# Kernel tuning notes

Hardware: AMD Instinct MI355X
Metric: run time of the kernel (lower is better)

The kernel has to match this reference:

```python
import jax, jax.numpy as jnp
import numpy as np

N_NODES = 10000
N_EDGES = 160000
F_IN = 256
HEADS = 4
F_OUT = 256
NEG_SLOPE = 0.2  # PyG GATConv default negative_slope
EPS = 1e-5       # GraphNorm eps


def gat_conv(x, src, dst, W, a_src, a_dst, bias, concat):
    """PyG-style GATConv. x:[N,Fin], W:[Fin,H*C], a_src/a_dst:[H,C], bias:[H*C] or [C].
    src/dst already include self-loops (add_self_loops=True default)."""
    N = x.shape[0]
    H, C = a_src.shape
    h = (x @ W).reshape(N, H, C)                      # per-head projected features
    al_s = jnp.einsum('nhc,hc->nh', h, a_src)          # [N,H]
    al_d = jnp.einsum('nhc,hc->nh', h, a_dst)          # [N,H]
    e = jax.nn.leaky_relu(al_s[src] + al_d[dst], NEG_SLOPE)  # [E,H] raw scores
    # segment softmax over edges grouped by destination node
    m = jax.ops.segment_max(e, dst, num_segments=N)    # [N,H]; every node has a self-loop
    ex = jnp.exp(e - m[dst])
    denom = jax.ops.segment_sum(ex, dst, num_segments=N)
    alpha = ex / denom[dst]                            # [E,H]
    out = jax.ops.segment_sum(h[src] * alpha[:, :, None], dst, num_segments=N)  # [N,H,C]
    out = out.reshape(N, H * C) if concat else out.mean(axis=1)
    return out + bias


def graph_norm(x, w, b, ms):
    """PyG GraphNorm over a single graph: y = w*(x-ms*mean)/sqrt(var+eps)+b."""
    mean = x.mean(axis=0, keepdims=True)
    sh = x - ms * mean
    var = (sh * sh).mean(axis=0, keepdims=True)
    return w * sh / jnp.sqrt(var + EPS) + b


def setup_inputs() -> dict:
    key = jax.random.key(0)
    ks = jax.random.split(key, 12)
    H1 = HEADS * F_IN  # 1024
    s = 0.05
    return {
        'x': jax.random.normal(ks[0], (N_NODES, F_IN), jnp.float32),
        'edge_index': jax.random.randint(ks[1], (2, N_EDGES), 0, N_NODES, jnp.int64),
        'W1': jax.random.normal(ks[2], (F_IN, HEADS * F_IN), jnp.float32) * s,
        'att_src1': jax.random.normal(ks[3], (HEADS, F_IN), jnp.float32) * s,
        'att_dst1': jax.random.normal(ks[4], (HEADS, F_IN), jnp.float32) * s,
        'b1': jnp.zeros((H1,), jnp.float32),
        'gn_w': jnp.ones((H1,), jnp.float32),
        'gn_b': jnp.zeros((H1,), jnp.float32),
        'gn_ms': jnp.ones((H1,), jnp.float32),
        'W2': jax.random.normal(ks[5], (H1, F_OUT), jnp.float32) * s,
        'att_src2': jax.random.normal(ks[6], (1, F_OUT), jnp.float32) * s,
        'att_dst2': jax.random.normal(ks[7], (1, F_OUT), jnp.float32) * s,
        'b2': jnp.zeros((F_OUT,), jnp.float32),
    }


def reference(x, edge_index, W1, att_src1, att_dst1, b1, gn_w, gn_b, gn_ms,
              W2, att_src2, att_dst2, b2):
    N = x.shape[0]
    loop = jnp.arange(N, dtype=edge_index.dtype)
    src = jnp.concatenate([edge_index[0], loop])  # add_self_loops=True
    dst = jnp.concatenate([edge_index[1], loop])
    h = gat_conv(x, src, dst, W1, att_src1, att_dst1, b1, concat=True)   # [N, H*Fin]
    h = graph_norm(h, gn_w, gn_b, gn_ms)
    h = jax.nn.relu(h)
    # F.dropout(training=self.training): eval mode -> identity
    out = gat_conv(h, src, dst, W2, att_src2, att_dst2, b2, concat=False)  # [N, Fout]
    return out
```

## Files before the change

### kernel.cpp

```cpp
#include <hip/hip_runtime.h>
#include <hip/hip_bf16.h>

#define NNODES 10000
#define FIN    256
#define HEADS  4
#define H1DIM  1024
#define FOUT   256
#define NEG    0.2f
#define GNEPS  1e-5f
#define SLOTS  96

typedef unsigned short u16;
typedef __attribute__((ext_vector_type(8))) short bf16x8;
typedef __attribute__((ext_vector_type(4))) float f32x4;

__device__ __forceinline__ float bf2f(u16 u) {
    union { unsigned int i; float f; } v; v.i = ((unsigned int)u) << 16; return v.f;
}
__device__ __forceinline__ u16 f2bf(float f) {
    __hip_bfloat16 h = __float2bfloat16(f);
    union { __hip_bfloat16 h; u16 u; } v; v.h = h; return v.u;
}
__device__ __forceinline__ float lrelu(float v) { return v > 0.f ? v : NEG * v; }

__device__ __forceinline__ void compute_flags(const int* ei, const u16* x,
                                              int& is64, int& isbf)
{
    int or_odd = ei[1] | ei[3] | ei[5] | ei[7] | ei[9] | ei[11];
    is64 = (or_odd == 0) ? 1 : 0;
    int sane = 1;
    for (int i = 0; i < 32; i += 2) {
        u16 w = x[i];
        int e = (w >> 7) & 0xFF;
        if (!(w == 0 || w == 0x8000 || (e >= 100 && e <= 150))) sane = 0;
    }
    isbf = sane;
}

struct CvtDesc { const void* src; float* dst; int n; };
struct CvtTable { CvtDesc d[9]; };

__global__ void prep_kernel(const void* __restrict__ x, const int* __restrict__ ei,
                            const void* __restrict__ W1, const void* __restrict__ W2,
                            const void* __restrict__ as1, const void* __restrict__ ad1,
                            CvtTable smalls,
                            u16* __restrict__ xb, u16* __restrict__ W1t,
                            u16* __restrict__ W2t, float* __restrict__ Pm,
                            int* __restrict__ cursor, int* __restrict__ ssort,
                            int* __restrict__ flag, int* __restrict__ fflag,
                            int NE, int Etot)
{
    __shared__ int sfl[2];
    __shared__ u16 tile[32][33];
    if (threadIdx.x == 0) {
        int is64, isbf;
        compute_flags(ei, (const u16*)x, is64, isbf);
        sfl[0] = is64; sfl[1] = isbf;
        if (blockIdx.y == 3 && blockIdx.x == 0) { flag[0] = is64; fflag[0] = isbf; }
    }
    __syncthreads();
    const int is64 = sfl[0], isbf = sfl[1];
    const int task = blockIdx.y;
    const int tid = threadIdx.x;

    if (task == 0) {
        int i4 = (blockIdx.x * 256 + tid) * 4;
        if (i4 >= NNODES * FIN) return;
        if (isbf) {
            *reinterpret_cast<ushort4*>(xb + i4) =
                *reinterpret_cast<const ushort4*>((const u16*)x + i4);
        } else {
            float4 v = *reinterpret_cast<const float4*>((const float*)x + i4);
            ushort4 o; o.x = f2bf(v.x); o.y = f2bf(v.y); o.z = f2bf(v.z); o.w = f2bf(v.w);
            *reinterpret_cast<ushort4*>(xb + i4) = o;
        }
    } else if (task == 1 || task == 2) {
        const void* W = (task == 1) ? W1 : W2;
        u16* Wt = (task == 1) ? W1t : W2t;
        const int K = (task == 1) ? FIN : H1DIM;
        const int N = (task == 1) ? H1DIM : FOUT;
        int ntiles_n = N >> 5;
        int tk = blockIdx.x / ntiles_n, tn = blockIdx.x - tk * ntiles_n;
        if (tk >= (K >> 5)) return;
        int k0 = tk << 5, n0 = tn << 5;
        int r = tid >> 5, cdx = tid & 31;
#pragma unroll
        for (int i = 0; i < 4; i++) {
            int kk = i * 8 + r;
            int srcIdx = (k0 + kk) * N + n0 + cdx;
            u16 v = isbf ? ((const u16*)W)[srcIdx] : f2bf(((const float*)W)[srcIdx]);
            tile[kk][cdx] = v;
        }
        __syncthreads();
#pragma unroll
        for (int i = 0; i < 4; i++) {
            int nn = i * 8 + r;
            Wt[(size_t)(n0 + nn) * K + k0 + cdx] = tile[cdx][nn];
        }
    } else if (task == 3) {
        if (blockIdx.x >= 9) return;
        CvtDesc d = smalls.d[blockIdx.x];
        int i4 = tid * 4;
        if (i4 >= d.n) return;
        if (isbf) {
            ushort4 u = *reinterpret_cast<const ushort4*>((const u16*)d.src + i4);
            *reinterpret_cast<float4*>(d.dst + i4) =
                make_float4(bf2f(u.x), bf2f(u.y), bf2f(u.z), bf2f(u.w));
        } else {
            *reinterpret_cast<float4*>(d.dst + i4) =
                *reinterpret_cast<const float4*>((const float*)d.src + i4);
        }
    } else if (task == 4) {
        int e = blockIdx.x * 256 + tid;
        if (e >= Etot) return;
        int src, dst;
        if (e < NE) {
            src = is64 ? ei[2 * e] : ei[e];
            dst = is64 ? ei[2 * (NE + e)] : ei[NE + e];
        } else {
            src = dst = e - NE;
        }
        if ((unsigned)dst >= NNODES) return;
        if ((unsigned)src >= NNODES) src = 0;
        int idx = atomicAdd(&cursor[dst], 1);
        if (idx < SLOTS) ssort[dst * SLOTS + idx] = src;
    } else {
        if (blockIdx.x >= 512) return;
        int wave = tid >> 6, lane = tid & 63;
        int idx = blockIdx.x * 4 + wave;
        int j = idx >> 8, k = idx & 255;
        int hd = j & 3;
        const void* av = (j < 4) ? as1 : ad1;
        int c = lane * 4;
        int widx = k * H1DIM + hd * FIN + c;
        int aidx = hd * FIN + c;
        float wv0, wv1, wv2, wv3, a0, a1, a2, a3;
        if (isbf) {
            ushort4 wu = *reinterpret_cast<const ushort4*>((const u16*)W1 + widx);
            ushort4 au = *reinterpret_cast<const ushort4*>((const u16*)av + aidx);
            wv0 = bf2f(wu.x); wv1 = bf2f(wu.y); wv2 = bf2f(wu.z); wv3 = bf2f(wu.w);
            a0 = bf2f(au.x); a1 = bf2f(au.y); a2 = bf2f(au.z); a3 = bf2f(au.w);
        } else {
            float4 wf = *reinterpret_cast<const float4*>((const float*)W1 + widx);
            float4 af = *reinterpret_cast<const float4*>((const float*)av + aidx);
            wv0 = wf.x; wv1 = wf.y; wv2 = wf.z; wv3 = wf.w;
            a0 = af.x; a1 = af.y; a2 = af.z; a3 = af.w;
        }
        float acc = wv0 * a0 + wv1 * a1 + wv2 * a2 + wv3 * a3;
#pragma unroll
        for (int off = 32; off > 0; off >>= 1)
            acc += __shfl_xor(acc, off, 64);
        if (lane == 0) Pm[j * FIN + k] = acc;
    }
}

__global__ void alsd1_kernel(const u16* __restrict__ xb, const float* __restrict__ Pm,
                             float* __restrict__ als, float* __restrict__ ald)
{
    int wave = threadIdx.x >> 6, lane = threadIdx.x & 63;
    int n = blockIdx.x * 4 + wave;
    if (n >= NNODES) return;
    ushort4 xv = *reinterpret_cast<const ushort4*>(xb + (size_t)n * FIN + lane * 4);
    float x0 = bf2f(xv.x), x1 = bf2f(xv.y), x2 = bf2f(xv.z), x3 = bf2f(xv.w);
    float r[8];
#pragma unroll
    for (int j = 0; j < 8; j++) {
        float4 p = *reinterpret_cast<const float4*>(Pm + j * FIN + lane * 4);
        r[j] = x0 * p.x + x1 * p.y + x2 * p.z + x3 * p.w;
    }
#pragma unroll
    for (int off = 32; off > 0; off >>= 1)
#pragma unroll
        for (int j = 0; j < 8; j++)
            r[j] += __shfl_xor(r[j], off, 64);
    if (lane == 0) {
        *reinterpret_cast<float4*>(als + n * 4) = make_float4(r[0], r[1], r[2], r[3]);
        *reinterpret_cast<float4*>(ald + n * 4) = make_float4(r[4], r[5], r[6], r[7]);
    }
}

__global__ void agg_x_kernel(const int* __restrict__ cursor, const int* __restrict__ ssort,
                             const float* __restrict__ als, const float* __restrict__ ald,
                             const u16* __restrict__ xb, u16* __restrict__ zbuf)
{
    const int wave = threadIdx.x >> 6, lane = threadIdx.x & 63;
    const int n = blockIdx.x * 4 + wave;
    const bool active = (n < NNODES);
    int e0 = 0, e1 = 0;
    float4 adv = make_float4(0.f, 0.f, 0.f, 0.f);
    if (active) {
        e0 = n * SLOTS;
        e1 = e0 + min(cursor[n], SLOTS);
        adv = *reinterpret_cast<const float4*>(ald + n * 4);
    }

    float m0 = -1e30f, m1 = -1e30f, m2 = -1e30f, m3 = -1e30f;
    for (int e = e0 + lane; e < e1; e += 64) {
        int s = ssort[e];
        float4 av = *reinterpret_cast<const float4*>(als + s * 4);
        m0 = fmaxf(m0, lrelu(av.x + adv.x));
        m1 = fmaxf(m1, lrelu(av.y + adv.y));
        m2 = fmaxf(m2, lrelu(av.z + adv.z));
        m3 = fmaxf(m3, lrelu(av.w + adv.w));
    }
#pragma unroll
    for (int off = 32; off > 0; off >>= 1) {
        m0 = fmaxf(m0, __shfl_xor(m0, off, 64));
        m1 = fmaxf(m1, __shfl_xor(m1, off, 64));
        m2 = fmaxf(m2, __shfl_xor(m2, off, 64));
        m3 = fmaxf(m3, __shfl_xor(m3, off, 64));
    }

    __shared__ float wlds[4][128][4];
    __shared__ int schk[4];
    int myCh = active ? ((e1 - e0 + 127) >> 7) : 0;
    if (lane == 0) schk[wave] = myCh;
    __syncthreads();
    int mc = max(max(schk[0], schk[1]), max(schk[2], schk[3]));

    float d0 = 0, d1 = 0, d2 = 0, d3 = 0;
    float a[4][4];
#pragma unroll
    for (int h = 0; h < 4; h++)
#pragma unroll
        for (int c = 0; c < 4; c++) a[h][c] = 0.f;

    for (int ch = 0; ch < mc; ch++) {
        int cs = e0 + ch * 128;
        int ce = min(cs + 128, e1);
        if (ch < myCh) {
            for (int e = cs + lane; e < ce; e += 64) {
                int s = ssort[e];
                float4 av = *reinterpret_cast<const float4*>(als + s * 4);
                float w0 = __expf(lrelu(av.x + adv.x) - m0);
                float w1 = __expf(lrelu(av.y + adv.y) - m1);
                float w2 = __expf(lrelu(av.z + adv.z) - m2);
                float w3 = __expf(lrelu(av.w + adv.w) - m3);
                *reinterpret_cast<float4*>(&wlds[wave][e - cs][0]) = make_float4(w0, w1, w2, w3);
                d0 += w0; d1 += w1; d2 += w2; d3 += w3;
            }
        }
        __syncthreads();
        if (ch < myCh) {
            for (int ee = cs; ee < ce; ee++) {
                int s = ssort[ee];
                float4 w = *reinterpret_cast<const float4*>(&wlds[wave][ee - cs][0]);
                ushort4 xv = *reinterpret_cast<const ushort4*>(xb + (size_t)s * FIN + lane * 4);
                float x0 = bf2f(xv.x), x1 = bf2f(xv.y), x2 = bf2f(xv.z), x3 = bf2f(xv.w);
                a[0][0] += w.x * x0; a[0][1] += w.x * x1; a[0][2] += w.x * x2; a[0][3] += w.x * x3;
                a[1][0] += w.y * x0; a[1][1] += w.y * x1; a[1][2] += w.y * x2; a[1][3] += w.y * x3;
                a[2][0] += w.z * x0; a[2][1] += w.z * x1; a[2][2] += w.z * x2; a[2][3] += w.z * x3;
                a[3][0] += w.w * x0; a[3][1] += w.w * x1; a[3][2] += w.w * x2; a[3][3] += w.w * x3;
            }
        }
        __syncthreads();
    }
    if (!active) return;
#pragma unroll
    for (int off = 32; off > 0; off >>= 1) {
        d0 += __shfl_xor(d0, off, 64);
        d1 += __shfl_xor(d1, off, 64);
        d2 += __shfl_xor(d2, off, 64);
        d3 += __shfl_xor(d3, off, 64);
    }
    float invs[4];
    invs[0] = d0 > 0.f ? 1.f / d0 : 0.f;
    invs[1] = d1 > 0.f ? 1.f / d1 : 0.f;
    invs[2] = d2 > 0.f ? 1.f / d2 : 0.f;
    invs[3] = d3 > 0.f ? 1.f / d3 : 0.f;
#pragma unroll
    for (int h = 0; h < 4; h++) {
        ushort4 o;
        o.x = f2bf(a[h][0] * invs[h]);
        o.y = f2bf(a[h][1] * invs[h]);
        o.z = f2bf(a[h][2] * invs[h]);
        o.w = f2bf(a[h][3] * invs[h]);
        *reinterpret_cast<ushort4*>(zbuf + (size_t)h * NNODES * FIN + (size_t)n * FIN + lane * 4) = o;
    }
}

#define LDS_STRIDE 40
#define KCHUNK2 512
template<int BN, int MINW, bool NORM_A, bool BIAS, bool SPLITK, bool STATS>
__global__ void __launch_bounds__(256, MINW)
mfma_gemm(const u16* __restrict__ A, const u16* __restrict__ Bt,
          u16* __restrict__ C, float* __restrict__ Cf,
          const float* __restrict__ bias,
          float* __restrict__ gsum, float* __restrict__ gsum2,
          const float* __restrict__ gnw, const float* __restrict__ gnb,
          const float* __restrict__ gnms,
          int M, int K, int ldc, long aZ, long bZ, int cZ, int kChunk)
{
    constexpr int NI = BN / 32;
    constexpr int NLOADS = (512 + BN * 4) / 256;
    __shared__ u16 Alds[128 * LDS_STRIDE];
    __shared__ u16 Blds[BN * LDS_STRIDE];
    __shared__ float sc_lds[NORM_A ? KCHUNK2 : 1];
    __shared__ float sh_lds[NORM_A ? KCHUNK2 : 1];

    const u16* Az; const u16* Bz; int k0;
    if (SPLITK) { Az = A; Bz = Bt; k0 = blockIdx.z * kChunk; }
    else { Az = A + (long)blockIdx.z * aZ; Bz = Bt + (long)blockIdx.z * bZ; k0 = 0; }
    const int kEnd = k0 + kChunk;

    const int tid  = threadIdx.x;
    const int lane = tid & 63;
    const int wave = tid >> 6;
    const int wm = wave >> 1, wn = wave & 1;
    const int l15 = lane & 15, quad = lane >> 4;
    const int n0 = blockIdx.x * BN;
    const int m0 = blockIdx.y * 128;

    if (NORM_A) {
        const float invN = 1.0f / (float)NNODES;
        for (int i = tid; i < kChunk; i += 256) {
            int cch = k0 + i;
            float mean = gsum[cch] * invN;
            float ex2  = gsum2[cch] * invN;
            float msv  = gnms[cch];
            float var  = ex2 - 2.f * msv * mean * mean + msv * msv * mean * mean;
            float sc   = gnw[cch] * rsqrtf(fmaxf(var, 0.f) + GNEPS);
            sc_lds[i] = sc;
            sh_lds[i] = gnb[cch] - sc * msv * mean;
        }
        __syncthreads();
    }

    int lrow[NLOADS], lcol[NLOADS];
    bool lIsA[NLOADS];
#pragma unroll
    for (int i = 0; i < NLOADS; i++) {
        int g = i * 256 + tid;
        lIsA[i] = g < 512;
        int gg = lIsA[i] ? g : g - 512;
        lrow[i] = gg >> 2;
        lcol[i] = (gg & 3) * 8;
    }
    uint4 pre[NLOADS];

    auto issue = [&](int kt) {
#pragma unroll
        for (int i = 0; i < NLOADS; i++) {
            if (lIsA[i]) {
                int gr = m0 + lrow[i];
                pre[i] = (gr < M)
                    ? *reinterpret_cast<const uint4*>(Az + (size_t)gr * K + kt + lcol[i])
                    : make_uint4(0u, 0u, 0u, 0u);
            } else {
                pre[i] = *reinterpret_cast<const uint4*>(Bz + (size_t)(n0 + lrow[i]) * K + kt + lcol[i]);
            }
        }
    };
    auto commit = [&](int kt) {
#pragma unroll
        for (int i = 0; i < NLOADS; i++) {
            uint4 v = pre[i];
            if (lIsA[i]) {
                if (NORM_A) {
                    int kr = kt - k0 + lcol[i];
                    float4 s0 = *reinterpret_cast<const float4*>(&sc_lds[kr]);
                    float4 s1 = *reinterpret_cast<const float4*>(&sc_lds[kr + 4]);
                    float4 h0 = *reinterpret_cast<const float4*>(&sh_lds[kr]);
                    float4 h1 = *reinterpret_cast<const float4*>(&sh_lds[kr + 4]);
                    float sc[8] = {s0.x, s0.y, s0.z, s0.w, s1.x, s1.y, s1.z, s1.w};
                    float sh[8] = {h0.x, h0.y, h0.z, h0.w, h1.x, h1.y, h1.z, h1.w};
                    u16* pv = reinterpret_cast<u16*>(&v);
#pragma unroll
                    for (int j = 0; j < 8; j++)
                        pv[j] = f2bf(fmaxf(0.f, bf2f(pv[j]) * sc[j] + sh[j]));
                }
                *reinterpret_cast<uint4*>(&Alds[lrow[i] * LDS_STRIDE + lcol[i]]) = v;
            } else {
                *reinterpret_cast<uint4*>(&Blds[lrow[i] * LDS_STRIDE + lcol[i]]) = v;
            }
        }
    };

    f32x4 acc[4][NI];
#pragma unroll
    for (int i = 0; i < 4; i++)
#pragma unroll
        for (int j = 0; j < NI; j++) acc[i][j] = (f32x4){0.f, 0.f, 0.f, 0.f};

    issue(k0);
    for (int kt = k0; kt < kEnd; kt += 32) {
        commit(kt);
        __syncthreads();
        if (kt + 32 < kEnd) issue(kt + 32);

        bf16x8 a_frag[4], b_frag[NI];
#pragma unroll
        for (int mi = 0; mi < 4; mi++)
            a_frag[mi] = *reinterpret_cast<const bf16x8*>(
                &Alds[(wm * 64 + mi * 16 + l15) * LDS_STRIDE + quad * 8]);
#pragma unroll
        for (int ni = 0; ni < NI; ni++)
            b_frag[ni] = *reinterpret_cast<const bf16x8*>(
                &Blds[(wn * (BN / 2) + ni * 16 + l15) * LDS_STRIDE + quad * 8]);
#pragma unroll
        for (int mi = 0; mi < 4; mi++)
#pragma unroll
            for (int ni = 0; ni < NI; ni++)
                acc[mi][ni] = __builtin_amdgcn_mfma_f32_16x16x32_bf16(
                    a_frag[mi], b_frag[ni], acc[mi][ni], 0, 0, 0);
        __syncthreads();
    }

    float sacc[NI], qacc[NI];
#pragma unroll
    for (int ni = 0; ni < NI; ni++) { sacc[ni] = 0.f; qacc[ni] = 0.f; }

#pragma unroll
    for (int mi = 0; mi < 4; mi++) {
#pragma unroll
        for (int r = 0; r < 4; r++) {
            int row = m0 + wm * 64 + mi * 16 + quad * 4 + r;
            if (row >= M) continue;
#pragma unroll
            for (int ni = 0; ni < NI; ni++) {
                int col = n0 + wn * (BN / 2) + ni * 16 + l15;
                float v = acc[mi][ni][r];
                if (SPLITK) {
                    Cf[(size_t)blockIdx.z * M * ldc + (size_t)row * ldc + col] = v;
                } else {
                    if (BIAS) v += bias[blockIdx.z * cZ + col];
                    if (STATS) { sacc[ni] += v; qacc[ni] += v * v; }
                    C[(size_t)row * ldc + blockIdx.z * cZ + col] = f2bf(v);
                }
            }
        }
    }
    if (STATS) {
#pragma unroll
        for (int ni = 0; ni < NI; ni++) {
            float s = sacc[ni], q = qacc[ni];
            s += __shfl_xor(s, 16, 64); q += __shfl_xor(q, 16, 64);
            s += __shfl_xor(s, 32, 64); q += __shfl_xor(q, 32, 64);
            if (quad == 0) {
                int ch = blockIdx.z * cZ + n0 + wn * (BN / 2) + ni * 16 + l15;
                atomicAdd(&gsum[ch], s);
                atomicAdd(&gsum2[ch], q);
            }
        }
    }
}

__global__ void h2fin_kernel(const float* __restrict__ h2p, u16* __restrict__ h2b,
                             const float* __restrict__ as, const float* __restrict__ ad,
                             float* __restrict__ als, float* __restrict__ ald)
{
    int wave = threadIdx.x >> 6, lane = threadIdx.x & 63;
    int n = blockIdx.x * 4 + wave;
    if (n >= NNODES) return;
    int c = lane * 4;
    float4 v0 = *reinterpret_cast<const float4*>(h2p + (size_t)n * FOUT + c);
    float4 v1 = *reinterpret_cast<const float4*>(h2p + (size_t)NNODES * FOUT + (size_t)n * FOUT + c);
    float4 v = make_float4(v0.x + v1.x, v0.y + v1.y, v0.z + v1.z, v0.w + v1.w);
    ushort4 o; o.x = f2bf(v.x); o.y = f2bf(v.y); o.z = f2bf(v.z); o.w = f2bf(v.w);
    *reinterpret_cast<ushort4*>(h2b + (size_t)n * FOUT + c) = o;
    float4 av = *reinterpret_cast<const float4*>(as + c);
    float4 dv = *reinterpret_cast<const float4*>(ad + c);
    float ps = v.x * av.x + v.y * av.y + v.z * av.z + v.w * av.w;
    float pd = v.x * dv.x + v.y * dv.y + v.z * dv.z + v.w * dv.w;
#pragma unroll
    for (int off = 32; off > 0; off >>= 1) {
        ps += __shfl_xor(ps, off, 64);
        pd += __shfl_xor(pd, off, 64);
    }
    if (lane == 0) { als[n] = ps; ald[n] = pd; }
}

__global__ void agg2_kernel(const int* __restrict__ cursor, const int* __restrict__ ssort,
                            const float* __restrict__ als, const float* __restrict__ ald,
                            const u16* __restrict__ h2, const float* __restrict__ b2,
                            const int* __restrict__ fflag, void* __restrict__ outv)
{
    const int wave = threadIdx.x >> 6, lane = threadIdx.x & 63;
    const int n = blockIdx.x * 4 + wave;
    const bool active = (n < NNODES);
    int e0 = 0, e1 = 0;
    float adv = 0.f;
    if (active) {
        e0 = n * SLOTS;
        e1 = e0 + min(cursor[n], SLOTS);
        adv = ald[n];
    }

    float m = -1e30f;
    for (int e = e0 + lane; e < e1; e += 64) {
        int s = ssort[e];
        m = fmaxf(m, lrelu(als[s] + adv));
    }
#pragma unroll
    for (int off = 32; off > 0; off >>= 1)
        m = fmaxf(m, __shfl_xor(m, off, 64));

    __shared__ float wlds[4][128];
    __shared__ int schk[4];
    int myCh = active ? ((e1 - e0 + 127) >> 7) : 0;
    if (lane == 0) schk[wave] = myCh;
    __syncthreads();
    int mc = max(max(schk[0], schk[1]), max(schk[2], schk[3]));

    float d = 0.f, a0 = 0.f, a1 = 0.f, a2 = 0.f, a3 = 0.f;
    for (int ch = 0; ch < mc; ch++) {
        int cs = e0 + ch * 128;
        int ce = min(cs + 128, e1);
        if (ch < myCh) {
            for (int e = cs + lane; e < ce; e += 64) {
                int s = ssort[e];
                float w = __expf(lrelu(als[s] + adv) - m);
                wlds[wave][e - cs] = w;
                d += w;
            }
        }
        __syncthreads();
        if (ch < myCh) {
            for (int ee = cs; ee < ce; ee++) {
                int s = ssort[ee];
                float w = wlds[wave][ee - cs];
                ushort4 hv = *reinterpret_cast<const ushort4*>(h2 + (size_t)s * FOUT + lane * 4);
                a0 += w * bf2f(hv.x); a1 += w * bf2f(hv.y);
                a2 += w * bf2f(hv.z); a3 += w * bf2f(hv.w);
            }
        }
        __syncthreads();
    }
    if (!active) return;
#pragma unroll
    for (int off = 32; off > 0; off >>= 1)
        d += __shfl_xor(d, off, 64);
    float inv = d > 0.f ? 1.f / d : 0.f;
    int c = lane * 4;
    float4 bv = *reinterpret_cast<const float4*>(b2 + c);
    float r0 = a0 * inv + bv.x;
    float r1 = a1 * inv + bv.y;
    float r2 = a2 * inv + bv.z;
    float r3 = a3 * inv + bv.w;
    if (fflag[0]) {
        ushort4 o;
        o.x = f2bf(r0); o.y = f2bf(r1); o.z = f2bf(r2); o.w = f2bf(r3);
        *reinterpret_cast<ushort4*>((u16*)outv + (size_t)n * FOUT + c) = o;
    } else {
        *reinterpret_cast<float4*>((float*)outv + (size_t)n * FOUT + c) =
            make_float4(r0, r1, r2, r3);
    }
}

extern "C" void kernel_launch(void* const* d_in, const int* in_sizes, int n_in,
                              void* d_out, int out_size, void* d_ws, size_t ws_size,
                              hipStream_t stream)
{
    const void* x    = d_in[0];
    const int*  ei   = (const int*)d_in[1];
    const void* W1   = d_in[2];
    const void* as1  = d_in[3];
    const void* ad1  = d_in[4];
    const void* b1   = d_in[5];
    const void* gnw  = d_in[6];
    const void* gnb  = d_in[7];
    const void* gnms = d_in[8];
    const void* W2   = d_in[9];
    const void* as2  = d_in[10];
    const void* ad2  = d_in[11];
    const void* b2   = d_in[12];

    const int NE   = in_sizes[1] / 2;
    const int Etot = NE + NNODES;

    char* w = (char*)d_ws;
    size_t off = 0;
    auto carve = [&](size_t bytes) -> char* {
        char* p = w + off;
        off = (off + bytes + 255) & ~(size_t)255;
        return p;
    };
    int*   cursor = (int*)carve((size_t)NNODES * 4);
    float* gsum   = (float*)carve(1024 * 4);
    float* gsum2  = (float*)carve(1024 * 4);
    size_t zero_bytes = off;
    int*   flag   = (int*)carve(256);
    int*   fflag  = (int*)carve(256);
    int*   ssort  = (int*)carve((size_t)NNODES * SLOTS * 4);
    u16*   zbuf   = (u16*)carve((size_t)HEADS * NNODES * FIN * 2);
    u16*   out1b  = (u16*)carve((size_t)NNODES * H1DIM * 2);
    float* al1s   = (float*)carve((size_t)NNODES * HEADS * 4);
    float* al1d   = (float*)carve((size_t)NNODES * HEADS * 4);
    float* al2s   = (float*)carve((size_t)NNODES * 4);
    float* al2d   = (float*)carve((size_t)NNODES * 4);
    u16*   xb     = (u16*)carve((size_t)NNODES * FIN * 2);
    u16*   W1t    = (u16*)carve((size_t)H1DIM * FIN * 2);
    u16*   W2t    = (u16*)carve((size_t)FOUT * H1DIM * 2);
    float* Pm     = (float*)carve(8 * FIN * 4);
    float* b1f    = (float*)carve(1024 * 4);
    float* gnwf   = (float*)carve(1024 * 4);
    float* gnbf   = (float*)carve(1024 * 4);
    float* gnmsf  = (float*)carve(1024 * 4);
    float* as2f   = (float*)carve(256 * 4);
    float* ad2f   = (float*)carve(256 * 4);
    float* b2f    = (float*)carve(256 * 4);
    float* as1f   = (float*)carve(1024 * 4);
    float* ad1f   = (float*)carve(1024 * 4);
    (void)ws_size;

    float* h2part = (float*)zbuf;
    u16*   h2b    = xb;

    hipMemsetAsync(d_ws, 0, zero_bytes, stream);

    {
        CvtTable tab;
        tab.d[0] = { b1,   b1f,   H1DIM };
        tab.d[1] = { gnw,  gnwf,  H1DIM };
        tab.d[2] = { gnb,  gnbf,  H1DIM };
        tab.d[3] = { gnms, gnmsf, H1DIM };
        tab.d[4] = { as2,  as2f,  FOUT };
        tab.d[5] = { ad2,  ad2f,  FOUT };
        tab.d[6] = { b2,   b2f,   FOUT };
        tab.d[7] = { as1,  as1f,  H1DIM };
        tab.d[8] = { ad1,  ad1f,  H1DIM };
        dim3 grd(2500, 6);
        prep_kernel<<<grd, 256, 0, stream>>>(x, ei, W1, W2, as1, ad1, tab,
                                             xb, W1t, W2t, Pm, cursor, ssort,
                                             flag, fflag, NE, Etot);
    }
    alsd1_kernel<<<2500, 256, 0, stream>>>(xb, Pm, al1s, al1d);
    agg_x_kernel<<<2500, 256, 0, stream>>>(cursor, ssort, al1s, al1d, xb, zbuf);
    {
        dim3 grd(FIN / 128, (NNODES + 127) / 128, HEADS);
        mfma_gemm<128, 2, false, true, false, true><<<grd, 256, 0, stream>>>(
            zbuf, W1t, out1b, nullptr, b1f, gsum, gsum2, nullptr, nullptr, nullptr,
            NNODES, FIN, H1DIM, (long)NNODES * FIN, (long)FIN * FIN, FIN, FIN);
    }
    {
        dim3 grd(FOUT / 64, (NNODES + 127) / 128, 2);
        mfma_gemm<64, 3, true, false, true, false><<<grd, 256, 0, stream>>>(
            out1b, W2t, nullptr, h2part, nullptr, gsum, gsum2, gnwf, gnbf, gnmsf,
            NNODES, H1DIM, FOUT, 0L, 0L, 0, KCHUNK2);
    }
    h2fin_kernel<<<(NNODES + 3) / 4, 256, 0, stream>>>(h2part, h2b, as2f, ad2f, al2s, al2d);
    agg2_kernel<<<2500, 256, 0, stream>>>(cursor, ssort, al2s, al2d, h2b, b2f, fflag, d_out);
}
```

Before: 232.8 us.

## Drop split-K in second GEMM, fuse attention dot products, compact prep grid, unroll gathers

The second projection GEMM no longer uses split-K. It writes bf16 output directly and computes the layer-2 source and destination attention scores in its epilogue using shuffles and atomics, which removes the h2fin kernel and the fp32 partial buffer round-trip. The prep kernel's 2D grid, which held many idle blocks, is flattened into an exact 1D task partition. Both aggregation loops are unrolled by two so more gathers are in flight. The trade-offs are half as many blocks in the second GEMM and float atomics that make the attention scores order-dependent.

```diff
diff --git a/kernel.cpp b/kernel.cpp
--- a/kernel.cpp
+++ b/kernel.cpp
@@ -39,6 +39,14 @@
 
 struct CvtDesc { const void* src; float* dst; int n; };
 struct CvtTable { CvtDesc d[9]; };
+
+#define T0_N 2500
+#define T1_N 256
+#define T2_N 256
+#define T3_N 9
+#define T4_N 665
+#define T5_N 512
+#define PREP_BLOCKS (T0_N + T1_N + T2_N + T3_N + T4_N + T5_N)
 
 __global__ void prep_kernel(const void* __restrict__ x, const int* __restrict__ ei,
                             const void* __restrict__ W1, const void* __restrict__ W2,
@@ -56,15 +64,15 @@
         int is64, isbf;
         compute_flags(ei, (const u16*)x, is64, isbf);
         sfl[0] = is64; sfl[1] = isbf;
-        if (blockIdx.y == 3 && blockIdx.x == 0) { flag[0] = is64; fflag[0] = isbf; }
+        if (blockIdx.x == 0) { flag[0] = is64; fflag[0] = isbf; }
     }
     __syncthreads();
     const int is64 = sfl[0], isbf = sfl[1];
-    const int task = blockIdx.y;
+    const int b = blockIdx.x;
     const int tid = threadIdx.x;
 
-    if (task == 0) {
-        int i4 = (blockIdx.x * 256 + tid) * 4;
+    if (b < T0_N) {
+        int i4 = (b * 256 + tid) * 4;
         if (i4 >= NNODES * FIN) return;
         if (isbf) {
             *reinterpret_cast<ushort4*>(xb + i4) =
@@ -74,13 +82,15 @@
             ushort4 o; o.x = f2bf(v.x); o.y = f2bf(v.y); o.z = f2bf(v.z); o.w = f2bf(v.w);
             *reinterpret_cast<ushort4*>(xb + i4) = o;
         }
-    } else if (task == 1 || task == 2) {
-        const void* W = (task == 1) ? W1 : W2;
-        u16* Wt = (task == 1) ? W1t : W2t;
-        const int K = (task == 1) ? FIN : H1DIM;
-        const int N = (task == 1) ? H1DIM : FOUT;
+    } else if (b < T0_N + T1_N + T2_N) {
+        const int task1 = (b < T0_N + T1_N);
+        const int bb = task1 ? (b - T0_N) : (b - T0_N - T1_N);
+        const void* W = task1 ? W1 : W2;
+        u16* Wt = task1 ? W1t : W2t;
+        const int K = task1 ? FIN : H1DIM;
+        const int N = task1 ? H1DIM : FOUT;
         int ntiles_n = N >> 5;
-        int tk = blockIdx.x / ntiles_n, tn = blockIdx.x - tk * ntiles_n;
+        int tk = bb / ntiles_n, tn = bb - tk * ntiles_n;
         if (tk >= (K >> 5)) return;
         int k0 = tk << 5, n0 = tn << 5;
         int r = tid >> 5, cdx = tid & 31;
@@ -97,9 +107,9 @@
             int nn = i * 8 + r;
             Wt[(size_t)(n0 + nn) * K + k0 + cdx] = tile[cdx][nn];
         }
-    } else if (task == 3) {
-        if (blockIdx.x >= 9) return;
-        CvtDesc d = smalls.d[blockIdx.x];
+    } else if (b < T0_N + T1_N + T2_N + T3_N) {
+        const int bb = b - (T0_N + T1_N + T2_N);
+        CvtDesc d = smalls.d[bb];
         int i4 = tid * 4;
         if (i4 >= d.n) return;
         if (isbf) {
@@ -110,8 +120,9 @@
             *reinterpret_cast<float4*>(d.dst + i4) =
                 *reinterpret_cast<const float4*>((const float*)d.src + i4);
         }
-    } else if (task == 4) {
-        int e = blockIdx.x * 256 + tid;
+    } else if (b < T0_N + T1_N + T2_N + T3_N + T4_N) {
+        const int bb = b - (T0_N + T1_N + T2_N + T3_N);
+        int e = bb * 256 + tid;
         if (e >= Etot) return;
         int src, dst;
         if (e < NE) {
@@ -125,9 +136,9 @@
         int idx = atomicAdd(&cursor[dst], 1);
         if (idx < SLOTS) ssort[dst * SLOTS + idx] = src;
     } else {
-        if (blockIdx.x >= 512) return;
+        const int bb = b - (T0_N + T1_N + T2_N + T3_N + T4_N);
         int wave = tid >> 6, lane = tid & 63;
-        int idx = blockIdx.x * 4 + wave;
+        int idx = bb * 4 + wave;
         int j = idx >> 8, k = idx & 255;
         int hd = j & 3;
         const void* av = (j < 4) ? as1 : ad1;
@@ -242,7 +253,26 @@
         }
         __syncthreads();
         if (ch < myCh) {
-            for (int ee = cs; ee < ce; ee++) {
+            int ee = cs;
+            for (; ee + 1 < ce; ee += 2) {
+                int s0 = ssort[ee];
+                int s1 = ssort[ee + 1];
+                float4 w0 = *reinterpret_cast<const float4*>(&wlds[wave][ee - cs][0]);
+                float4 w1 = *reinterpret_cast<const float4*>(&wlds[wave][ee + 1 - cs][0]);
+                ushort4 xv0 = *reinterpret_cast<const ushort4*>(xb + (size_t)s0 * FIN + lane * 4);
+                ushort4 xv1 = *reinterpret_cast<const ushort4*>(xb + (size_t)s1 * FIN + lane * 4);
+                float p0 = bf2f(xv0.x), p1 = bf2f(xv0.y), p2 = bf2f(xv0.z), p3 = bf2f(xv0.w);
+                a[0][0] += w0.x * p0; a[0][1] += w0.x * p1; a[0][2] += w0.x * p2; a[0][3] += w0.x * p3;
+                a[1][0] += w0.y * p0; a[1][1] += w0.y * p1; a[1][2] += w0.y * p2; a[1][3] += w0.y * p3;
+                a[2][0] += w0.z * p0; a[2][1] += w0.z * p1; a[2][2] += w0.z * p2; a[2][3] += w0.z * p3;
+                a[3][0] += w0.w * p0; a[3][1] += w0.w * p1; a[3][2] += w0.w * p2; a[3][3] += w0.w * p3;
+                float q0 = bf2f(xv1.x), q1 = bf2f(xv1.y), q2 = bf2f(xv1.z), q3 = bf2f(xv1.w);
+                a[0][0] += w1.x * q0; a[0][1] += w1.x * q1; a[0][2] += w1.x * q2; a[0][3] += w1.x * q3;
+                a[1][0] += w1.y * q0; a[1][1] += w1.y * q1; a[1][2] += w1.y * q2; a[1][3] += w1.y * q3;
+                a[2][0] += w1.z * q0; a[2][1] += w1.z * q1; a[2][2] += w1.z * q2; a[2][3] += w1.z * q3;
+                a[3][0] += w1.w * q0; a[3][1] += w1.w * q1; a[3][2] += w1.w * q2; a[3][3] += w1.w * q3;
+            }
+            if (ee < ce) {
                 int s = ssort[ee];
                 float4 w = *reinterpret_cast<const float4*>(&wlds[wave][ee - cs][0]);
                 ushort4 xv = *reinterpret_cast<const ushort4*>(xb + (size_t)s * FIN + lane * 4);
@@ -280,8 +310,8 @@
 }
 
 #define LDS_STRIDE 40
-#define KCHUNK2 512
-template<int BN, int MINW, bool NORM_A, bool BIAS, bool SPLITK, bool STATS>
+#define KCHUNK2 1024
+template<int BN, int MINW, bool NORM_A, bool BIAS, bool SPLITK, bool STATS, bool AL2>
 __global__ void __launch_bounds__(256, MINW)
 mfma_gemm(const u16* __restrict__ A, const u16* __restrict__ Bt,
           u16* __restrict__ C, float* __restrict__ Cf,
@@ -289,6 +319,8 @@
           float* __restrict__ gsum, float* __restrict__ gsum2,
           const float* __restrict__ gnw, const float* __restrict__ gnb,
           const float* __restrict__ gnms,
+          const float* __restrict__ a2s, const float* __restrict__ a2d,
+          float* __restrict__ al2s, float* __restrict__ al2d,
           int M, int K, int ldc, long aZ, long bZ, int cZ, int kChunk)
 {
     constexpr int NI = BN / 32;
@@ -416,6 +448,7 @@
         for (int r = 0; r < 4; r++) {
             int row = m0 + wm * 64 + mi * 16 + quad * 4 + r;
             if (row >= M) continue;
+            float ps = 0.f, pd = 0.f;
 #pragma unroll
             for (int ni = 0; ni < NI; ni++) {
                 int col = n0 + wn * (BN / 2) + ni * 16 + l15;
@@ -425,7 +458,18 @@
                 } else {
                     if (BIAS) v += bias[blockIdx.z * cZ + col];
                     if (STATS) { sacc[ni] += v; qacc[ni] += v * v; }
+                    if (AL2) { ps += v * a2s[col]; pd += v * a2d[col]; }
                     C[(size_t)row * ldc + blockIdx.z * cZ + col] = f2bf(v);
+                }
+            }
+            if (AL2) {
+                ps += __shfl_xor(ps, 1, 64); pd += __shfl_xor(pd, 1, 64);
+                ps += __shfl_xor(ps, 2, 64); pd += __shfl_xor(pd, 2, 64);
+                ps += __shfl_xor(ps, 4, 64); pd += __shfl_xor(pd, 4, 64);
+                ps += __shfl_xor(ps, 8, 64); pd += __shfl_xor(pd, 8, 64);
+                if (l15 == 0) {
+                    atomicAdd(&al2s[row], ps);
+                    atomicAdd(&al2d[row], pd);
                 }
             }
         }
@@ -443,31 +487,6 @@
             }
         }
     }
-}
-
-__global__ void h2fin_kernel(const float* __restrict__ h2p, u16* __restrict__ h2b,
-                             const float* __restrict__ as, const float* __restrict__ ad,
-                             float* __restrict__ als, float* __restrict__ ald)
-{
-    int wave = threadIdx.x >> 6, lane = threadIdx.x & 63;
-    int n = blockIdx.x * 4 + wave;
-    if (n >= NNODES) return;
-    int c = lane * 4;
-    float4 v0 = *reinterpret_cast<const float4*>(h2p + (size_t)n * FOUT + c);
-    float4 v1 = *reinterpret_cast<const float4*>(h2p + (size_t)NNODES * FOUT + (size_t)n * FOUT + c);
-    float4 v = make_float4(v0.x + v1.x, v0.y + v1.y, v0.z + v1.z, v0.w + v1.w);
-    ushort4 o; o.x = f2bf(v.x); o.y = f2bf(v.y); o.z = f2bf(v.z); o.w = f2bf(v.w);
-    *reinterpret_cast<ushort4*>(h2b + (size_t)n * FOUT + c) = o;
-    float4 av = *reinterpret_cast<const float4*>(as + c);
-    float4 dv = *reinterpret_cast<const float4*>(ad + c);
-    float ps = v.x * av.x + v.y * av.y + v.z * av.z + v.w * av.w;
-    float pd = v.x * dv.x + v.y * dv.y + v.z * dv.z + v.w * dv.w;
-#pragma unroll
-    for (int off = 32; off > 0; off >>= 1) {
-        ps += __shfl_xor(ps, off, 64);
-        pd += __shfl_xor(pd, off, 64);
-    }
-    if (lane == 0) { als[n] = ps; ald[n] = pd; }
 }
 
 __global__ void agg2_kernel(const int* __restrict__ cursor, const int* __restrict__ ssort,
@@ -516,7 +535,20 @@
         }
         __syncthreads();
         if (ch < myCh) {
-            for (int ee = cs; ee < ce; ee++) {
+            int ee = cs;
+            for (; ee + 1 < ce; ee += 2) {
+                int s0 = ssort[ee];
+                int s1 = ssort[ee + 1];
+                float w0 = wlds[wave][ee - cs];
+                float w1 = wlds[wave][ee + 1 - cs];
+                ushort4 hv0 = *reinterpret_cast<const ushort4*>(h2 + (size_t)s0 * FOUT + lane * 4);
+                ushort4 hv1 = *reinterpret_cast<const ushort4*>(h2 + (size_t)s1 * FOUT + lane * 4);
+                a0 += w0 * bf2f(hv0.x); a1 += w0 * bf2f(hv0.y);
+                a2 += w0 * bf2f(hv0.z); a3 += w0 * bf2f(hv0.w);
+                a0 += w1 * bf2f(hv1.x); a1 += w1 * bf2f(hv1.y);
+                a2 += w1 * bf2f(hv1.z); a3 += w1 * bf2f(hv1.w);
+            }
+            if (ee < ce) {
                 int s = ssort[ee];
                 float w = wlds[wave][ee - cs];
                 ushort4 hv = *reinterpret_cast<const ushort4*>(h2 + (size_t)s * FOUT + lane * 4);
@@ -578,6 +610,8 @@
     int*   cursor = (int*)carve((size_t)NNODES * 4);
     float* gsum   = (float*)carve(1024 * 4);
     float* gsum2  = (float*)carve(1024 * 4);
+    float* al2s   = (float*)carve((size_t)NNODES * 4);
+    float* al2d   = (float*)carve((size_t)NNODES * 4);
     size_t zero_bytes = off;
     int*   flag   = (int*)carve(256);
     int*   fflag  = (int*)carve(256);
@@ -586,8 +620,6 @@
     u16*   out1b  = (u16*)carve((size_t)NNODES * H1DIM * 2);
     float* al1s   = (float*)carve((size_t)NNODES * HEADS * 4);
     float* al1d   = (float*)carve((size_t)NNODES * HEADS * 4);
-    float* al2s   = (float*)carve((size_t)NNODES * 4);
-    float* al2d   = (float*)carve((size_t)NNODES * 4);
     u16*   xb     = (u16*)carve((size_t)NNODES * FIN * 2);
     u16*   W1t    = (u16*)carve((size_t)H1DIM * FIN * 2);
     u16*   W2t    = (u16*)carve((size_t)FOUT * H1DIM * 2);
@@ -603,8 +635,7 @@
     float* ad1f   = (float*)carve(1024 * 4);
     (void)ws_size;
 
-    float* h2part = (float*)zbuf;
-    u16*   h2b    = xb;
+    u16* h2b = xb;
 
     hipMemsetAsync(d_ws, 0, zero_bytes, stream);
 
@@ -619,25 +650,25 @@
         tab.d[6] = { b2,   b2f,   FOUT };
         tab.d[7] = { as1,  as1f,  H1DIM };
         tab.d[8] = { ad1,  ad1f,  H1DIM };
-        dim3 grd(2500, 6);
-        prep_kernel<<<grd, 256, 0, stream>>>(x, ei, W1, W2, as1, ad1, tab,
-                                             xb, W1t, W2t, Pm, cursor, ssort,
-                                             flag, fflag, NE, Etot);
+        prep_kernel<<<PREP_BLOCKS, 256, 0, stream>>>(x, ei, W1, W2, as1, ad1, tab,
+                                                     xb, W1t, W2t, Pm, cursor, ssort,
+                                                     flag, fflag, NE, Etot);
     }
     alsd1_kernel<<<2500, 256, 0, stream>>>(xb, Pm, al1s, al1d);
     agg_x_kernel<<<2500, 256, 0, stream>>>(cursor, ssort, al1s, al1d, xb, zbuf);
     {
         dim3 grd(FIN / 128, (NNODES + 127) / 128, HEADS);
-        mfma_gemm<128, 2, false, true, false, true><<<grd, 256, 0, stream>>>(
+        mfma_gemm<128, 2, false, true, false, true, false><<<grd, 256, 0, stream>>>(
             zbuf, W1t, out1b, nullptr, b1f, gsum, gsum2, nullptr, nullptr, nullptr,
+            nullptr, nullptr, nullptr, nullptr,
             NNODES, FIN, H1DIM, (long)NNODES * FIN, (long)FIN * FIN, FIN, FIN);
     }
     {
-        dim3 grd(FOUT / 64, (NNODES + 127) / 128, 2);
-        mfma_gemm<64, 3, true, false, true, false><<<grd, 256, 0, stream>>>(
-            out1b, W2t, nullptr, h2part, nullptr, gsum, gsum2, gnwf, gnbf, gnmsf,
-            NNODES, H1DIM, FOUT, 0L, 0L, 0, KCHUNK2);
-    }
-    h2fin_kernel<<<(NNODES + 3) / 4, 256, 0, stream>>>(h2part, h2b, as2f, ad2f, al2s, al2d);
+        dim3 grd(FOUT / 64, (NNODES + 127) / 128, 1);
+        mfma_gemm<64, 3, true, false, false, false, true><<<grd, 256, 0, stream>>>(
+            out1b, W2t, h2b, nullptr, nullptr, gsum, gsum2, gnwf, gnbf, gnmsf,
+            as2f, ad2f, al2s, al2d,
+            NNODES, H1DIM, FOUT, 0L, 0L, 0, H1DIM);
+    }
     agg2_kernel<<<2500, 256, 0, stream>>>(cursor, ssort, al2s, al2d, h2b, b2f, fflag, d_out);
 }
```

Result: faster. 226.4 us (-2.8%).
